# Performance work log

Measured on AMD Instinct MI355X. Metric: run time of the kernel, lower is better.

Reference implementation:

```python
import jax, jax.numpy as jnp
import numpy as np

B, C, D, H, W = 2, 16, 16, 128, 128
CO = 16            # out_channels
C8 = max(C // 8, 1)  # q/k channel dim in CC_module
EPS = 1e-5


def conv3d(x, w, pad):
    # x: [B,C,D,H,W], w: [O,I,kd,kh,kw]
    return jax.lax.conv_general_dilated(
        x, w, (1, 1, 1), [(p, p) for p in pad],
        dimension_numbers=('NCDHW', 'OIDHW', 'NCDHW'))


def bn5d(x, g, b, m, v):
    # eval-mode BatchNorm3d over channel axis 1
    sh = (1, -1, 1, 1, 1)
    return (x - m.reshape(sh)) * (g / jnp.sqrt(v + EPS)).reshape(sh) + b.reshape(sh)


def cc_attention(x, wq, wk, wv, gamma):
    # Criss-cross attention on one depth slice. x: [B,C,H,W]
    q = jnp.einsum('oc,bchw->bohw', wq, x)   # [B,C8,H,W]
    k = jnp.einsum('oc,bchw->bohw', wk, x)   # [B,C8,H,W]
    v = jnp.einsum('oc,bchw->bohw', wv, x)   # [B,C,H,W]
    Hh = x.shape[2]
    # column (H) attention energies, diagonal masked with -inf (CCNet INF trick)
    eH = jnp.einsum('bchw,bcjw->bhwj', q, k)                 # [B,H,W,H]
    eye = jnp.eye(Hh, dtype=bool)[None, :, None, :]
    eH = jnp.where(eye, -jnp.inf, eH)
    # row (W) attention energies
    eW = jnp.einsum('bchw,bchv->bhwv', q, k)                 # [B,H,W,W]
    att = jax.nn.softmax(jnp.concatenate([eH, eW], axis=-1), axis=-1)
    aH, aW = att[..., :Hh], att[..., Hh:]
    oH = jnp.einsum('bhwj,bcjw->bchw', aH, v)
    oW = jnp.einsum('bhwv,bchv->bchw', aW, v)
    return gamma * (oH + oW) + x


def setup_inputs() -> dict:
    key = jax.random.key(0)
    ks = jax.random.split(key, 12)
    f = lambda k, shp, s=0.05: jax.random.normal(k, shp, jnp.float32) * s
    return {
        'x': jax.random.normal(ks[0], (B, C, D, H, W), jnp.float32),
        # Conv3dBNReLU (k=(1,3,3), p=(0,1,1))
        'w_pre': f(ks[1], (C, C, 1, 3, 3)),
        'bn_pre_g': jnp.ones((C,), jnp.float32),
        'bn_pre_b': jnp.zeros((C,), jnp.float32),
        'bn_pre_m': f(ks[2], (C,)),
        'bn_pre_v': jax.random.uniform(ks[3], (C,), jnp.float32, 0.5, 1.5),
        # CC_module params (1x1 convs as matrices)
        'w_q': f(ks[4], (C8, C), 0.2),
        'w_k': f(ks[5], (C8, C), 0.2),
        'w_v': f(ks[6], (C, C), 0.2),
        'cc_gamma': jnp.asarray(0.1, jnp.float32),
        # gate conv BasicConv3d: C -> 4*CO, k=3,s=1,p=1, conv+BN
        'w_gate': f(ks[7], (4 * CO, C, 3, 3, 3)),
        'bn_g': jnp.ones((4 * CO,), jnp.float32),
        'bn_b': jnp.zeros((4 * CO,), jnp.float32),
        'bn_m': f(ks[8], (4 * CO,)),
        'bn_v': jax.random.uniform(ks[9], (4 * CO,), jnp.float32, 0.5, 1.5),
    }


def reference(x, w_pre, bn_pre_g, bn_pre_b, bn_pre_m, bn_pre_v,
              w_q, w_k, w_v, cc_gamma,
              w_gate, bn_g, bn_b, bn_m, bn_v):
    # Conv3dBNReLU
    x = jax.nn.relu(bn5d(conv3d(x, w_pre, (0, 1, 1)),
                         bn_pre_g, bn_pre_b, bn_pre_m, bn_pre_v))
    # criss-cross attention applied twice per depth slice (j in range(2))
    cc2 = lambda xs: cc_attention(
        cc_attention(xs, w_q, w_k, w_v, cc_gamma), w_q, w_k, w_v, cc_gamma)
    x = jax.vmap(cc2, in_axes=2, out_axes=2)(x)
    # SRU gates: conv to 4*CO channels, BN, split, nonlinearities
    gates = bn5d(conv3d(x, w_gate, (1, 1, 1)), bn_g, bn_b, bn_m, bn_v)
    Wx, ft, rt, X = jnp.split(gates, 4, axis=1)
    Wx = jnp.tanh(Wx)
    ft = jax.nn.sigmoid(ft)
    rt = jax.nn.sigmoid(rt)
    X = jnp.tanh(X)  # act == 'tanh'
    # recurrence over depth axis via scan
    Wx_s, ft_s, rt_s, X_s = (jnp.moveaxis(t, 2, 0) for t in (Wx, ft, rt, X))
    C0 = 1.0 - ft_s[0]                        # first step: Ct = 1 - ft
    h0 = rt_s[0] * C0 + (1.0 - rt_s[0]) * X_s[0]

    def step(Ct, inp):
        wx_, ft_, rt_, x_ = inp
        Ct = ft_ * Ct + (1.0 - ft_) * wx_
        ht = rt_ * Ct + (1.0 - rt_) * x_
        return Ct, ht

    _, hts = jax.lax.scan(step, C0, (Wx_s[1:], ft_s[1:], rt_s[1:], X_s[1:]))
    hts = jnp.concatenate([h0[None], hts], axis=0)  # [D,B,CO,H,W]
    return jnp.moveaxis(hts, 0, 2)                  # [B,CO,D,H,W]
```

## Files before the change

kernel.cpp:

```cpp
#include <hip/hip_runtime.h>
#include <math.h>

namespace {
constexpr int B = 2, C = 16, D = 16, H = 128, W = 128;
constexpr int HW   = H * W;
constexpr int DHW  = D * HW;
constexpr int CDHW = C * DHW;
constexpr float EPSBN = 1e-5f;

constexpr long long OFF_R0  = 0;
constexpr long long OFF_R1  = 8388608;
constexpr long long OFF_K   = 16777216;
constexpr long long OFF_KT  = 17825792;
constexpr long long OFF_QT  = 18874368;
constexpr long long OFF_MST = 19922944;
constexpr long long OFF_SO  = 20447232;
constexpr long long OFF_R2  = 20971520;
constexpr long long OFF_R3  = 29360128;
}

using frag_ab = __attribute__((ext_vector_type(8))) short;
using frag_cd = __attribute__((ext_vector_type(4))) float;

__device__ __forceinline__ unsigned short f2bf(float f) {
  unsigned u = __float_as_uint(f);
  u = (u + 0x7FFF + ((u >> 16) & 1)) >> 16;
  return (unsigned short)u;
}
__device__ __forceinline__ float bf2f(short s) {
  return __uint_as_float(((unsigned)(unsigned short)s) << 16);
}
__device__ __forceinline__ unsigned cvt_pk_bf16(float lo, float hi) {
  unsigned r;
  asm volatile("v_cvt_pk_bf16_f32 %0, %1, %2" : "=v"(r) : "v"(lo), "v"(hi));
  return r;
}

__global__ __launch_bounds__(256) void k_x16(
    const float* __restrict__ x, short* __restrict__ XB0)
{
  const int tid = threadIdx.x;
  const int tile = blockIdx.x, d = blockIdx.y, b = blockIdx.z;
  const int h0 = (tile >> 3) * 16, w0 = (tile & 7) * 16;
  const long long xbase = (long long)b * CDHW + (long long)d * HW;
  const int th = tid >> 4, tw = tid & 15;

  float v[16];
  #pragma unroll
  for (int c = 0; c < 16; ++c)
    v[c] = x[xbase + (long long)c * DHW + (h0 + th) * 128 + (w0 + tw)];

  unsigned pk[8];
  #pragma unroll
  for (int c = 0; c < 8; ++c)
    pk[c] = (unsigned)f2bf(v[2 * c]) | ((unsigned)f2bf(v[2 * c + 1]) << 16);
  short* dst = XB0 + ((long long)(b * D + d) * HW + (h0 + th) * 128 + (w0 + tw)) * 16;
  *(uint4*)(dst)     = make_uint4(pk[0], pk[1], pk[2], pk[3]);
  *(uint4*)(dst + 8) = make_uint4(pk[4], pk[5], pk[6], pk[7]);
}

__global__ __launch_bounds__(256) void k_wp(
    const float* __restrict__ wp, short* __restrict__ WP16)
{
  const int idx = blockIdx.x * 256 + threadIdx.x;
  if (idx >= 2 * 16 * 96) return;
  const int u = idx / 96;
  const int k = idx - u * 96;
  const int ks = k >> 5, rem = k & 31;
  const int t = rem >> 3, c8 = rem & 7;
  const int tap = ks * 4 + t;
  const int half = u >> 4, co = u & 15;
  const int cin = half * 8 + c8;
  float v = (tap < 9) ? wp[co * 144 + cin * 9 + tap] : 0.f;
  WP16[idx] = (short)f2bf(v);
}

__global__ __launch_bounds__(256) void k_conv_pre16(
    const short* __restrict__ XB0, const short* __restrict__ WP16,
    const float* __restrict__ bg, const float* __restrict__ bb,
    const float* __restrict__ bm, const float* __restrict__ bv,
    float* __restrict__ X1)
{
  __shared__ short xls[10 * 132 * 8];
  const int tid = threadIdx.x;
  const int rg = blockIdx.x;
  const int d = blockIdx.y, b = blockIdx.z;
  const int h0 = rg * 8;

  const int lane = tid & 63;
  const int wv   = tid >> 6;
  const int p    = lane & 15;
  const int chunk = lane >> 4;

  const short* xb0 = XB0 + (long long)(b * D + d) * HW * 16;
  const frag_ab zero8 = {0, 0, 0, 0, 0, 0, 0, 0};

  frag_cd acc[2][8];
  #pragma unroll
  for (int r2 = 0; r2 < 2; ++r2)
    #pragma unroll
    for (int pg = 0; pg < 8; ++pg)
      acc[r2][pg] = (frag_cd){0.f, 0.f, 0.f, 0.f};

  int offs[3];
  #pragma unroll
  for (int s = 0; s < 3; ++s) {
    int tap = s * 4 + chunk;
    if (tap > 8) tap = 0;
    const int kh = (tap * 11) >> 5;
    const int kw = tap - kh * 3;
    offs[s] = ((2 * wv + kh) * 132 + p + kw) * 8;
  }

  for (int half = 0; half < 2; ++half) {
    for (int idx = tid; idx < 1320; idx += 256) {
      const int row = idx / 132, col = idx - row * 132;
      const int gh = h0 - 1 + row, gw = col - 1;
      frag_ab v = zero8;
      if (gh >= 0 && gh < H && gw >= 0 && gw < W)
        v = *(const frag_ab*)(xb0 + ((long long)gh * 128 + gw) * 16 + half * 8);
      *(frag_ab*)&xls[idx * 8] = v;
    }
    __syncthreads();

    frag_ab a[3];
    {
      const short* wl = WP16 + ((half << 4) + p) * 96 + chunk * 8;
      #pragma unroll
      for (int s = 0; s < 3; ++s)
        a[s] = *(const frag_ab*)(wl + s * 32);
    }

    #pragma unroll
    for (int s = 0; s < 3; ++s) {
      const frag_ab av = a[s];
      const int base0 = offs[s];
      #pragma unroll
      for (int pg = 0; pg < 8; ++pg) {
        frag_ab b0 = *(const frag_ab*)&xls[base0 + pg * 128];
        acc[0][pg] = __builtin_amdgcn_mfma_f32_16x16x32_bf16(av, b0, acc[0][pg], 0, 0, 0);
        frag_ab b1 = *(const frag_ab*)&xls[base0 + 1056 + pg * 128];
        acc[1][pg] = __builtin_amdgcn_mfma_f32_16x16x32_bf16(av, b1, acc[1][pg], 0, 0, 0);
      }
    }
    __syncthreads();
  }

  float sc4[4], bi4[4];
  #pragma unroll
  for (int reg = 0; reg < 4; ++reg) {
    const int co = chunk * 4 + reg;
    float s = bg[co] * rsqrtf(bv[co] + EPSBN);
    sc4[reg] = s;
    bi4[reg] = bb[co] - bm[co] * s;
  }
  const long long xbase = (long long)b * CDHW + (long long)d * HW;
  #pragma unroll
  for (int r2 = 0; r2 < 2; ++r2) {
    const int row = h0 + 2 * wv + r2;
    #pragma unroll
    for (int pg = 0; pg < 8; ++pg)
      #pragma unroll
      for (int reg = 0; reg < 4; ++reg) {
        const int co = chunk * 4 + reg;
        float v = fmaxf(fmaf(acc[r2][pg][reg], sc4[reg], bi4[reg]), 0.f);
        X1[xbase + (long long)co * DHW + row * 128 + pg * 16 + p] = v;
      }
  }
}

__global__ __launch_bounds__(256) void k_qkv(
    const float* __restrict__ xin, const float* __restrict__ wq,
    const float* __restrict__ wk, const float* __restrict__ wv,
    float* __restrict__ Kp, float* __restrict__ KTp, float* __restrict__ QTp,
    short* __restrict__ Vp16, short* __restrict__ VTp16)
{
  const int tid = threadIdx.x;
  const int tile = blockIdx.x, d = blockIdx.y, b = blockIdx.z;
  const int h0 = (tile >> 3) * 16, w0 = (tile & 7) * 16;
  const int ty = tid >> 4, tx = tid & 15;
  const int h = h0 + ty, w = w0 + tx;

  const float* xb = xin + (long long)b * CDHW + (long long)d * HW + h * 128 + w;
  float xv[16];
  #pragma unroll
  for (int c = 0; c < 16; ++c) xv[c] = xb[(long long)c * DHW];

  float q0 = 0, q1 = 0, k0 = 0, k1 = 0, v[16];
  #pragma unroll
  for (int c = 0; c < 16; ++c) {
    q0 = fmaf(wq[c], xv[c], q0);
    q1 = fmaf(wq[16 + c], xv[c], q1);
    k0 = fmaf(wk[c], xv[c], k0);
    k1 = fmaf(wk[16 + c], xv[c], k1);
  }
  #pragma unroll
  for (int o = 0; o < 16; ++o) {
    float a = 0;
    #pragma unroll
    for (int c = 0; c < 16; ++c) a = fmaf(wv[o * 16 + c], xv[c], a);
    v[o] = a;
  }

  const int sl = b * 16 + d;
  const long long base2 = (long long)(sl * 2) * HW;
  const long long baseV = (long long)(sl * 16) * HW;
  const int hw = h * 128 + w;
  Kp[base2 + hw] = k0;
  Kp[base2 + HW + hw] = k1;
  #pragma unroll
  for (int o = 0; o < 16; ++o)
    Vp16[baseV + (long long)o * HW + hw] = (short)f2bf(v[o]);

  __shared__ float lsk[2][16][17];
  __shared__ float lsq[2][16][17];
  __shared__ float lsv[16][16][17];
  lsk[0][ty][tx] = k0; lsk[1][ty][tx] = k1;
  lsq[0][ty][tx] = q0; lsq[1][ty][tx] = q1;
  #pragma unroll
  for (int o = 0; o < 16; ++o) lsv[o][ty][tx] = v[o];
  __syncthreads();

  const int wh = (w0 + ty) * 128 + (h0 + tx);
  KTp[base2 + wh]      = lsk[0][tx][ty];
  KTp[base2 + HW + wh] = lsk[1][tx][ty];
  QTp[base2 + wh]      = lsq[0][tx][ty];
  QTp[base2 + HW + wh] = lsq[1][tx][ty];
  #pragma unroll
  for (int o = 0; o < 16; ++o)
    VTp16[baseV + (long long)o * HW + wh] = (short)f2bf(lsv[o][tx][ty]);
}

template<bool MASK_INNER>
__global__ __launch_bounds__(256) void k_att_row(
    const float* __restrict__ xin, float* __restrict__ OWn,
    const float* __restrict__ Kp, const short* __restrict__ Vp16,
    float* __restrict__ Sip, const float* __restrict__ wq)
{
  __shared__ float kr2[4][128][2];
  __shared__ float q0l[4][128], q1l[4][128];
  __shared__ __align__(16) short v16[4][16][136];
  const int tid = threadIdx.x;
  const int o0 = blockIdx.x * 4, d = blockIdx.y, b = blockIdx.z;
  const int sl = b * 16 + d;
  const long long base2 = (long long)(sl * 2) * HW;
  const long long baseV = (long long)(sl * 16) * HW;
  const long long baseM = (long long)sl * HW;
  const int hi = tid >> 6;
  const int L  = tid & 63;
  const int p  = L & 15;
  const int chunk = L >> 4;
  const int orow = o0 + hi;
  const long long xbase = (long long)b * CDHW + (long long)d * HW;

  for (int kk = tid; kk < 1024; kk += 256) {
    int col = kk & 127;
    int t = kk >> 7;
    int r2 = t >> 1, o = t & 1;
    kr2[r2][col][o] = Kp[base2 + (long long)o * HW + (o0 + r2) * 128 + col];
  }
  for (int idx = tid; idx < 2048; idx += 256) {
    int v4 = idx & 31;
    int t = idx >> 5;
    int c = t & 15, r2 = t >> 4;
    *(uint2*)&v16[r2][c][v4 * 4] =
        *(const uint2*)&Vp16[baseV + (long long)c * HW + (o0 + r2) * 128 + v4 * 4];
  }
  {
    float q0a = 0.f, q0b = 0.f, q1a = 0.f, q1b = 0.f;
    #pragma unroll
    for (int c = 0; c < 16; ++c) {
      const float w0 = wq[c], w1 = wq[16 + c];
      float xa = xin[xbase + (long long)c * DHW + orow * 128 + L];
      float xb2 = xin[xbase + (long long)c * DHW + orow * 128 + L + 64];
      q0a = fmaf(w0, xa, q0a);  q1a = fmaf(w1, xa, q1a);
      q0b = fmaf(w0, xb2, q0b); q1b = fmaf(w1, xb2, q1b);
    }
    q0l[hi][L] = q0a; q0l[hi][L + 64] = q0b;
    q1l[hi][L] = q1a; q1l[hi][L + 64] = q1b;
  }
  __syncthreads();

  float q0r[8], q1r[8];
  #pragma unroll
  for (int ti = 0; ti < 8; ++ti) {
    q0r[ti] = q0l[hi][ti * 16 + p];
    q1r[ti] = q1l[hi][ti * 16 + p];
  }

  frag_cd acc[8];
  #pragma unroll
  for (int ti = 0; ti < 8; ++ti) acc[ti] = (frag_cd){0.f, 0.f, 0.f, 0.f};
  float ssum[8] = {0.f, 0.f, 0.f, 0.f, 0.f, 0.f, 0.f, 0.f};

  #pragma unroll
  for (int ks = 0; ks < 4; ++ks) {
    const int vb = ks * 32 + chunk * 8;
    float2 kv[8];
    const float* kvp = &kr2[hi][vb][0];
    *(float4*)&kv[0] = *(const float4*)(kvp);
    *(float4*)&kv[2] = *(const float4*)(kvp + 4);
    *(float4*)&kv[4] = *(const float4*)(kvp + 8);
    *(float4*)&kv[6] = *(const float4*)(kvp + 12);
    frag_ab bfrag = *(const frag_ab*)&v16[hi][p][vb];

    #pragma unroll
    for (int ti = 0; ti < 8; ++ti) {
      float pv[8];
      #pragma unroll
      for (int j = 0; j < 8; ++j) {
        float e = fmaf(q0r[ti], kv[j].x, q1r[ti] * kv[j].y);
        pv[j] = __expf(e);
      }
      if constexpr (MASK_INNER) {
        const int dj = ti * 16 + p - vb;
        #pragma unroll
        for (int j = 0; j < 8; ++j)
          if (j == dj) pv[j] = 0.f;
      }
      float lsum = 0.f;
      #pragma unroll
      for (int j = 0; j < 8; ++j) lsum += pv[j];
      ssum[ti] += lsum;

      union { frag_ab f; unsigned u[4]; } cv;
      cv.u[0] = cvt_pk_bf16(pv[0], pv[1]);
      cv.u[1] = cvt_pk_bf16(pv[2], pv[3]);
      cv.u[2] = cvt_pk_bf16(pv[4], pv[5]);
      cv.u[3] = cvt_pk_bf16(pv[6], pv[7]);
      acc[ti] = __builtin_amdgcn_mfma_f32_16x16x32_bf16(cv.f, bfrag, acc[ti], 0, 0, 0);
    }
  }

  #pragma unroll
  for (int ti = 0; ti < 8; ++ti) {
    ssum[ti] += __shfl_xor(ssum[ti], 16);
    ssum[ti] += __shfl_xor(ssum[ti], 32);
  }
  if (L < 16) {
    #pragma unroll
    for (int ti = 0; ti < 8; ++ti)
      Sip[baseM + (ti * 16 + L) * 128 + orow] = ssum[ti];
  }

  float* ob = OWn + ((long long)(b * D + d) * HW + orow * 128) * 16;
  #pragma unroll
  for (int ti = 0; ti < 8; ++ti)
    #pragma unroll
    for (int reg = 0; reg < 4; ++reg)
      ob[(ti * 16 + chunk * 4 + reg) * 16 + p] = acc[ti][reg];
}

template<bool MASK_INNER>
__global__ __launch_bounds__(256) void k_att_col(
    const float* __restrict__ KTp, const float* __restrict__ QTp,
    const short* __restrict__ VTp16, float* __restrict__ OHn,
    float* __restrict__ Sop)
{
  __shared__ float kr2[4][128][2];
  __shared__ __align__(16) short v16[4][16][136];
  const int tid = threadIdx.x;
  const int i0 = blockIdx.x * 4, d = blockIdx.y, b = blockIdx.z;
  const int sl = b * 16 + d;
  const long long base2 = (long long)(sl * 2) * HW;
  const long long baseV = (long long)(sl * 16) * HW;
  const long long baseS = (long long)sl * HW;
  const int hi = tid >> 6;
  const int L  = tid & 63;
  const int p  = L & 15;
  const int chunk = L >> 4;
  const int icol = i0 + hi;

  for (int kk = tid; kk < 1024; kk += 256) {
    int col = kk & 127;
    int t = kk >> 7;
    int r2 = t >> 1, o = t & 1;
    kr2[r2][col][o] = KTp[base2 + (long long)o * HW + (i0 + r2) * 128 + col];
  }
  for (int idx = tid; idx < 2048; idx += 256) {
    int j4 = idx & 31;
    int t = idx >> 5;
    int c = t & 15, r2 = t >> 4;
    *(uint2*)&v16[r2][c][j4 * 4] =
        *(const uint2*)&VTp16[baseV + (long long)c * HW + (i0 + r2) * 128 + j4 * 4];
  }
  __syncthreads();

  float q0r[8], q1r[8];
  #pragma unroll
  for (int ti = 0; ti < 8; ++ti) {
    q0r[ti] = QTp[base2 + icol * 128 + ti * 16 + p];
    q1r[ti] = QTp[base2 + HW + icol * 128 + ti * 16 + p];
  }

  frag_cd acc[8];
  #pragma unroll
  for (int ti = 0; ti < 8; ++ti) acc[ti] = (frag_cd){0.f, 0.f, 0.f, 0.f};
  float ssum[8] = {0.f, 0.f, 0.f, 0.f, 0.f, 0.f, 0.f, 0.f};

  #pragma unroll
  for (int ks = 0; ks < 4; ++ks) {
    const int vb = ks * 32 + chunk * 8;
    float2 kv[8];
    const float* kvp = &kr2[hi][vb][0];
    *(float4*)&kv[0] = *(const float4*)(kvp);
    *(float4*)&kv[2] = *(const float4*)(kvp + 4);
    *(float4*)&kv[4] = *(const float4*)(kvp + 8);
    *(float4*)&kv[6] = *(const float4*)(kvp + 12);
    frag_ab bfrag = *(const frag_ab*)&v16[hi][p][vb];

    #pragma unroll
    for (int ti = 0; ti < 8; ++ti) {
      float pv[8];
      #pragma unroll
      for (int j = 0; j < 8; ++j) {
        float e = fmaf(q0r[ti], kv[j].x, q1r[ti] * kv[j].y);
        pv[j] = __expf(e);
      }
      if constexpr (!MASK_INNER) {
        const int dj = ti * 16 + p - vb;
        #pragma unroll
        for (int j = 0; j < 8; ++j)
          if (j == dj) pv[j] = 0.f;
      }
      float lsum = 0.f;
      #pragma unroll
      for (int j = 0; j < 8; ++j) lsum += pv[j];
      ssum[ti] += lsum;

      union { frag_ab f; unsigned u[4]; } cv;
      cv.u[0] = cvt_pk_bf16(pv[0], pv[1]);
      cv.u[1] = cvt_pk_bf16(pv[2], pv[3]);
      cv.u[2] = cvt_pk_bf16(pv[4], pv[5]);
      cv.u[3] = cvt_pk_bf16(pv[6], pv[7]);
      acc[ti] = __builtin_amdgcn_mfma_f32_16x16x32_bf16(cv.f, bfrag, acc[ti], 0, 0, 0);
    }
  }

  #pragma unroll
  for (int ti = 0; ti < 8; ++ti) {
    ssum[ti] += __shfl_xor(ssum[ti], 16);
    ssum[ti] += __shfl_xor(ssum[ti], 32);
  }
  if (L < 16) {
    #pragma unroll
    for (int ti = 0; ti < 8; ++ti)
      Sop[baseS + icol * 128 + ti * 16 + L] = ssum[ti];
  }

  float* ob = OHn + ((long long)(b * D + d) * HW + icol * 128) * 16;
  #pragma unroll
  for (int ti = 0; ti < 8; ++ti)
    #pragma unroll
    for (int reg = 0; reg < 4; ++reg)
      ob[(ti * 16 + chunk * 4 + reg) * 16 + p] = acc[ti][reg];
}

template<bool TO_BF16>
__global__ __launch_bounds__(256) void k_comb(
    const float* __restrict__ Xn, const float* __restrict__ OWn,
    const float* __restrict__ OHn, const float* __restrict__ Sip,
    const float* __restrict__ Sop, const float* __restrict__ gp,
    float* __restrict__ Yt, short* __restrict__ Xb16)
{
  __shared__ float xs[16][16][17], ows[16][16][17];
  const int tid = threadIdx.x;
  const int tile = blockIdx.x, d = blockIdx.y, b = blockIdx.z;
  const int o0 = (tile >> 3) * 16, i0 = (tile & 7) * 16;
  const int sl = b * 16 + d;
  const long long baseM = (long long)sl * HW;
  const long long xbase = (long long)b * CDHW + (long long)d * HW;

  const int to = tid >> 4, ti = tid & 15;
  #pragma unroll
  for (int c = 0; c < 16; ++c) {
    const long long src = xbase + (long long)c * DHW + (o0 + to) * 128 + (i0 + ti);
    xs[c][to][ti] = Xn[src];
  }
  {
    const float* osrc = OWn + ((long long)(b * D + d) * HW + (o0 + to) * 128 + (i0 + ti)) * 16;
    float4 f0 = *(const float4*)(osrc);
    float4 f1 = *(const float4*)(osrc + 4);
    float4 f2 = *(const float4*)(osrc + 8);
    float4 f3 = *(const float4*)(osrc + 12);
    ows[0][to][ti] = f0.x;  ows[1][to][ti] = f0.y;
    ows[2][to][ti] = f0.z;  ows[3][to][ti] = f0.w;
    ows[4][to][ti] = f1.x;  ows[5][to][ti] = f1.y;
    ows[6][to][ti] = f1.z;  ows[7][to][ti] = f1.w;
    ows[8][to][ti] = f2.x;  ows[9][to][ti] = f2.y;
    ows[10][to][ti] = f2.z; ows[11][to][ti] = f2.w;
    ows[12][to][ti] = f3.x; ows[13][to][ti] = f3.y;
    ows[14][to][ti] = f3.z; ows[15][to][ti] = f3.w;
  }
  __syncthreads();

  const int ti2 = tid >> 4, to2 = tid & 15;
  const int i = i0 + ti2, o = o0 + to2;
  const float si = Sip[baseM + i * 128 + o];
  const float so = Sop[baseM + i * 128 + o];
  const float gi = gp[0] / (si + so);

  float oh[16];
  {
    const float* osrc = OHn + ((long long)(b * D + d) * HW + i * 128 + o) * 16;
    float4 f0 = *(const float4*)(osrc);
    float4 f1 = *(const float4*)(osrc + 4);
    float4 f2 = *(const float4*)(osrc + 8);
    float4 f3 = *(const float4*)(osrc + 12);
    oh[0] = f0.x;  oh[1] = f0.y;  oh[2] = f0.z;  oh[3] = f0.w;
    oh[4] = f1.x;  oh[5] = f1.y;  oh[6] = f1.z;  oh[7] = f1.w;
    oh[8] = f2.x;  oh[9] = f2.y;  oh[10] = f2.z; oh[11] = f2.w;
    oh[12] = f3.x; oh[13] = f3.y; oh[14] = f3.z; oh[15] = f3.w;
  }

  float res[16];
  #pragma unroll
  for (int c = 0; c < 16; ++c)
    res[c] = fmaf(gi, ows[c][to2][ti2] + oh[c], xs[c][to2][ti2]);

  if constexpr (!TO_BF16) {
    #pragma unroll
    for (int c = 0; c < 16; ++c)
      Yt[xbase + (long long)c * DHW + i * 128 + o] = res[c];
  } else {
    unsigned pk[8];
    #pragma unroll
    for (int c = 0; c < 8; ++c)
      pk[c] = (unsigned)f2bf(res[2 * c]) | ((unsigned)f2bf(res[2 * c + 1]) << 16);
    short* dst = Xb16 + ((long long)(b * D + d) * HW + i * 128 + o) * 16;
    *(uint4*)(dst)     = make_uint4(pk[0], pk[1], pk[2], pk[3]);
    *(uint4*)(dst + 8) = make_uint4(pk[4], pk[5], pk[6], pk[7]);
  }
}

__global__ __launch_bounds__(256) void k_wt(
    const float* __restrict__ wg, short* __restrict__ WT16)
{
  const int idx = blockIdx.x * 256 + threadIdx.x;
  if (idx >= 2 * 64 * 224) return;
  const int u = idx / 224;
  const int k = idx - u * 224;
  const int ks = k >> 5, rem = k & 31;
  const int t = rem >> 3, c8 = rem & 7;
  const int tap = ks * 4 + t;
  const int half = u >> 6, co = u & 63;
  const int cin = half * 8 + c8;
  float v = (tap < 27) ? wg[co * 432 + cin * 27 + tap] : 0.f;
  WT16[idx] = (short)f2bf(v);
}

__global__ __launch_bounds__(256, 2) void k_gates(
    const short* __restrict__ XB16, const short* __restrict__ WT16,
    short* __restrict__ g0, short* __restrict__ g1,
    short* __restrict__ g2, short* __restrict__ g3)
{
  __shared__ short xls[1584 * 8];
  const int tid = threadIdx.x;
  const int rp = blockIdx.x;
  const int d = blockIdx.y, b = blockIdx.z;
  const int h0 = rp * 2;

  const int lane = tid & 63;
  const int og   = tid >> 6;
  const int p    = lane & 15;
  const int chunk = lane >> 4;

  const short* xb = XB16 + (long long)(b * D) * HW * 16;
  const frag_ab zero8 = {0, 0, 0, 0, 0, 0, 0, 0};

  frag_cd acc[2][8];
  #pragma unroll
  for (int r2 = 0; r2 < 2; ++r2)
    #pragma unroll
    for (int pg = 0; pg < 8; ++pg)
      acc[r2][pg] = (frag_cd){0.f, 0.f, 0.f, 0.f};

  int offs[7];
  #pragma unroll
  for (int s = 0; s < 7; ++s) {
    int tap = s * 4 + chunk;
    if (tap > 26) tap = 0;
    const int kd = (tap * 57) >> 9;
    const int rem = tap - kd * 9;
    const int kh = (rem * 11) >> 5;
    const int kw = rem - kh * 3;
    offs[s] = ((kd * 4 + kh) * 132 + p + kw) * 8;
  }

  for (int half = 0; half < 2; ++half) {
    for (int idx = tid; idx < 1584; idx += 256) {
      const int kd = idx / 528;
      const int rem = idx - kd * 528;
      const int rr = rem / 132;
      const int col = rem - rr * 132;
      const int dd = d - 1 + kd, gh = h0 - 1 + rr, gw = col - 1;
      frag_ab v = zero8;
      if (dd >= 0 && dd < D && gh >= 0 && gh < H && gw >= 0 && gw < W)
        v = *(const frag_ab*)(xb + ((long long)dd * HW + gh * W + gw) * 16 + half * 8);
      *(frag_ab*)&xls[idx * 8] = v;
    }
    __syncthreads();

    frag_ab a[7];
    {
      const short* wl = WT16 + ((half << 6) + og * 16 + p) * 224 + chunk * 8;
      #pragma unroll
      for (int s = 0; s < 7; ++s)
        a[s] = *(const frag_ab*)(wl + s * 32);
    }

    #pragma unroll
    for (int s = 0; s < 7; ++s) {
      const frag_ab av = a[s];
      const int base0 = offs[s];
      #pragma unroll
      for (int pg = 0; pg < 8; ++pg) {
        frag_ab b0 = *(const frag_ab*)&xls[base0 + pg * 128];
        acc[0][pg] = __builtin_amdgcn_mfma_f32_16x16x32_bf16(av, b0, acc[0][pg], 0, 0, 0);
        frag_ab b1 = *(const frag_ab*)&xls[base0 + 1056 + pg * 128];
        acc[1][pg] = __builtin_amdgcn_mfma_f32_16x16x32_bf16(av, b1, acc[1][pg], 0, 0, 0);
      }
    }
    __syncthreads();
  }

  short* gbuf = (og == 0) ? g0 : (og == 1) ? g1 : (og == 2) ? g2 : g3;
  const long long base = (long long)b * CDHW + (long long)d * HW + h0 * W;
  #pragma unroll
  for (int r2 = 0; r2 < 2; ++r2)
    #pragma unroll
    for (int pg = 0; pg < 8; ++pg)
      #pragma unroll
      for (int reg = 0; reg < 4; ++reg) {
        const int cc = chunk * 4 + reg;
        gbuf[base + (long long)cc * DHW + r2 * W + pg * 16 + p] =
            (short)f2bf(acc[r2][pg][reg]);
      }
}

__global__ __launch_bounds__(256) void k_scan(
    const short* __restrict__ g0, const short* __restrict__ g1,
    const short* __restrict__ g2, const short* __restrict__ g3,
    const float* __restrict__ bg, const float* __restrict__ bb,
    const float* __restrict__ bm, const float* __restrict__ bv,
    float* __restrict__ out)
{
  const int g = blockIdx.x * 256 + threadIdx.x;
  const int hw = g & 16383;
  const int cc = (g >> 14) & 15;
  const int b  = g >> 18;

  float sc[4], bi[4];
  #pragma unroll
  for (int gg = 0; gg < 4; ++gg) {
    int ch = gg * 16 + cc;
    float s = bg[ch] * rsqrtf(bv[ch] + EPSBN);
    sc[gg] = s;
    bi[gg] = bb[ch] - bm[ch] * s;
  }

  const long long base = (long long)b * CDHW + (long long)cc * DHW + hw;
  float Ct = 0.f;
  for (int d = 0; d < D; ++d) {
    const long long idx = base + (long long)d * HW;
    float wx = tanhf(fmaf(bf2f(g0[idx]), sc[0], bi[0]));
    float ft = 1.f / (1.f + __expf(-fmaf(bf2f(g1[idx]), sc[1], bi[1])));
    float rt = 1.f / (1.f + __expf(-fmaf(bf2f(g2[idx]), sc[2], bi[2])));
    float xg = tanhf(fmaf(bf2f(g3[idx]), sc[3], bi[3]));
    Ct = (d == 0) ? (1.f - ft) : fmaf(ft, Ct, (1.f - ft) * wx);
    out[idx] = fmaf(rt, Ct, (1.f - rt) * xg);
  }
}

extern "C" void kernel_launch(void* const* d_in, const int* in_sizes, int n_in,
                              void* d_out, int out_size, void* d_ws, size_t ws_size,
                              hipStream_t stream) {
  const float* x      = (const float*)d_in[0];
  const float* w_pre  = (const float*)d_in[1];
  const float* bnpg   = (const float*)d_in[2];
  const float* bnpb   = (const float*)d_in[3];
  const float* bnpm   = (const float*)d_in[4];
  const float* bnpv   = (const float*)d_in[5];
  const float* wq     = (const float*)d_in[6];
  const float* wk     = (const float*)d_in[7];
  const float* wv     = (const float*)d_in[8];
  const float* gamma  = (const float*)d_in[9];
  const float* w_gate = (const float*)d_in[10];
  const float* bng    = (const float*)d_in[11];
  const float* bnb    = (const float*)d_in[12];
  const float* bnm    = (const float*)d_in[13];
  const float* bnv    = (const float*)d_in[14];

  float* ws  = (float*)d_ws;
  float* R0  = ws + OFF_R0;
  float* R1  = ws + OFF_R1;
  float* Kb  = ws + OFF_K;
  float* KTb = ws + OFF_KT;
  float* QTb = ws + OFF_QT;
  float* SI  = ws + OFF_MST;
  float* SO  = ws + OFF_SO;
  float* R2  = ws + OFF_R2;
  float* R3  = ws + OFF_R3;
  short* XB0  = (short*)(ws + OFF_R1);
  short* XB16 = (short*)(ws + OFF_R1);
  short* WP16 = (short*)(ws + OFF_SO);
  short* WT16 = (short*)(ws + OFF_K);
  short* V1b  = (short*)(ws + OFF_R2);
  short* VT1b = (short*)(ws + OFF_R3);
  short* V2b  = (short*)(ws + OFF_R0);
  short* VT2b = (short*)(ws + OFF_R1) + 8388608;
  short* G0b = (short*)(ws + OFF_R0);
  short* G1b = (short*)(ws + OFF_R0) + 8388608;
  short* G2b = (short*)(ws + OFF_R2);
  short* G3b = (short*)(ws + OFF_R2) + 8388608;
  float* out = (float*)d_out;

  const dim3 gTile(64, D, B), gAtt(32, D, B);

  k_wp <<<dim3(12),  dim3(256), 0, stream>>>(w_pre, WP16);
  k_x16<<<gTile,     dim3(256), 0, stream>>>(x, XB0);
  k_conv_pre16<<<dim3(16, D, B), dim3(256), 0, stream>>>(
      XB0, WP16, bnpg, bnpb, bnpm, bnpv, R0);

  k_qkv<<<gTile, dim3(256), 0, stream>>>(R0, wq, wk, wv, Kb, KTb, QTb, V1b, VT1b);
  k_att_row<false><<<gAtt, dim3(256), 0, stream>>>(R0, R1, Kb, V1b, SI, wq);
  k_att_col<false><<<gAtt, dim3(256), 0, stream>>>(KTb, QTb, VT1b, R2, SO);
  k_comb<false><<<gTile, dim3(256), 0, stream>>>(R0, R1, R2, SI, SO, gamma, R3, nullptr);

  k_qkv<<<gTile, dim3(256), 0, stream>>>(R3, wq, wk, wv, Kb, KTb, QTb, V2b, VT2b);
  k_att_row<true><<<gAtt, dim3(256), 0, stream>>>(R3, R2, Kb, V2b, SI, wq);
  k_att_col<true><<<gAtt, dim3(256), 0, stream>>>(KTb, QTb, VT2b, R0, SO);
  k_comb<true><<<gTile, dim3(256), 0, stream>>>(R3, R2, R0, SI, SO, gamma, nullptr, XB16);

  k_wt<<<dim3(112), dim3(256), 0, stream>>>(w_gate, WT16);

  k_gates<<<dim3(64, D, B), dim3(256), 0, stream>>>(XB16, WT16, G0b, G1b, G2b, G3b);

  k_scan<<<dim3(2048), dim3(256), 0, stream>>>(G0b, G1b, G2b, G3b, bng, bnb, bnm, bnv, out);
}
```

Measured before the change: 297.8 us.

## Store attention outputs as bf16 and fuse first combine with second QKV projection

Row and column attention outputs are now written as bf16 instead of fp32, halving those intermediate buffers' traffic. The first combine kernel also computes the q/k/v projections and their transposed copies for the second criss-cross pass, which removes one launch and one full re-read of the intermediate activation. Workspace aliasing is reshuffled to fit the new buffers. The cost is extra bf16 rounding on attention outputs and more registers and shared memory in the fused kernel.

```diff
diff --git a/kernel.cpp b/kernel.cpp
--- a/kernel.cpp
+++ b/kernel.cpp
@@ -233,7 +233,7 @@
 
 template<bool MASK_INNER>
 __global__ __launch_bounds__(256) void k_att_row(
-    const float* __restrict__ xin, float* __restrict__ OWn,
+    const float* __restrict__ xin, short* __restrict__ OWn16,
     const float* __restrict__ Kp, const short* __restrict__ Vp16,
     float* __restrict__ Sip, const float* __restrict__ wq)
 {
@@ -343,18 +343,18 @@
       Sip[baseM + (ti * 16 + L) * 128 + orow] = ssum[ti];
   }
 
-  float* ob = OWn + ((long long)(b * D + d) * HW + orow * 128) * 16;
+  short* ob = OWn16 + ((long long)(b * D + d) * HW + orow * 128) * 16;
   #pragma unroll
   for (int ti = 0; ti < 8; ++ti)
     #pragma unroll
     for (int reg = 0; reg < 4; ++reg)
-      ob[(ti * 16 + chunk * 4 + reg) * 16 + p] = acc[ti][reg];
+      ob[(ti * 16 + chunk * 4 + reg) * 16 + p] = (short)f2bf(acc[ti][reg]);
 }
 
 template<bool MASK_INNER>
 __global__ __launch_bounds__(256) void k_att_col(
     const float* __restrict__ KTp, const float* __restrict__ QTp,
-    const short* __restrict__ VTp16, float* __restrict__ OHn,
+    const short* __restrict__ VTp16, short* __restrict__ OHn16,
     float* __restrict__ Sop)
 {
   __shared__ float kr2[4][128][2];
@@ -448,20 +448,130 @@
       Sop[baseS + icol * 128 + ti * 16 + L] = ssum[ti];
   }
 
-  float* ob = OHn + ((long long)(b * D + d) * HW + icol * 128) * 16;
+  short* ob = OHn16 + ((long long)(b * D + d) * HW + icol * 128) * 16;
   #pragma unroll
   for (int ti = 0; ti < 8; ++ti)
     #pragma unroll
     for (int reg = 0; reg < 4; ++reg)
-      ob[(ti * 16 + chunk * 4 + reg) * 16 + p] = acc[ti][reg];
-}
-
-template<bool TO_BF16>
-__global__ __launch_bounds__(256) void k_comb(
-    const float* __restrict__ Xn, const float* __restrict__ OWn,
-    const float* __restrict__ OHn, const float* __restrict__ Sip,
+      ob[(ti * 16 + chunk * 4 + reg) * 16 + p] = (short)f2bf(acc[ti][reg]);
+}
+
+__global__ __launch_bounds__(256) void k_comb_qkv(
+    const float* __restrict__ Xn, const short* __restrict__ OWn16,
+    const short* __restrict__ OHn16, const float* __restrict__ Sip,
     const float* __restrict__ Sop, const float* __restrict__ gp,
-    float* __restrict__ Yt, short* __restrict__ Xb16)
+    const float* __restrict__ wq, const float* __restrict__ wk,
+    const float* __restrict__ wv,
+    float* __restrict__ Yt, float* __restrict__ Kp, float* __restrict__ KTp,
+    float* __restrict__ QTp, short* __restrict__ Vp16, short* __restrict__ VTp16)
+{
+  __shared__ float xs[16][16][17];
+  __shared__ float ows[16][16][17];
+  __shared__ float lsk[2][16][17], lsq[2][16][17];
+  const int tid = threadIdx.x;
+  const int tile = blockIdx.x, d = blockIdx.y, b = blockIdx.z;
+  const int o0 = (tile >> 3) * 16, i0 = (tile & 7) * 16;
+  const int sl = b * 16 + d;
+  const long long baseM = (long long)sl * HW;
+  const long long base2 = (long long)(sl * 2) * HW;
+  const long long baseV = (long long)(sl * 16) * HW;
+  const long long xbase = (long long)b * CDHW + (long long)d * HW;
+
+  const int to = tid >> 4, ti = tid & 15;
+  #pragma unroll
+  for (int c = 0; c < 16; ++c) {
+    const long long src = xbase + (long long)c * DHW + (o0 + to) * 128 + (i0 + ti);
+    xs[c][to][ti] = Xn[src];
+  }
+  {
+    const short* osrc = OWn16 + ((long long)(b * D + d) * HW + (o0 + to) * 128 + (i0 + ti)) * 16;
+    frag_ab f0 = *(const frag_ab*)(osrc);
+    frag_ab f1 = *(const frag_ab*)(osrc + 8);
+    #pragma unroll
+    for (int c = 0; c < 8; ++c) {
+      ows[c][to][ti]     = bf2f(f0[c]);
+      ows[c + 8][to][ti] = bf2f(f1[c]);
+    }
+  }
+  __syncthreads();
+
+  const int ti2 = tid >> 4, to2 = tid & 15;
+  const int i = i0 + ti2, o = o0 + to2;
+  const float si = Sip[baseM + i * 128 + o];
+  const float so = Sop[baseM + i * 128 + o];
+  const float gi = gp[0] / (si + so);
+
+  float oh[16];
+  {
+    const short* osrc = OHn16 + ((long long)(b * D + d) * HW + i * 128 + o) * 16;
+    frag_ab f0 = *(const frag_ab*)(osrc);
+    frag_ab f1 = *(const frag_ab*)(osrc + 8);
+    #pragma unroll
+    for (int c = 0; c < 8; ++c) { oh[c] = bf2f(f0[c]); oh[c + 8] = bf2f(f1[c]); }
+  }
+
+  float res[16];
+  #pragma unroll
+  for (int c = 0; c < 16; ++c)
+    res[c] = fmaf(gi, ows[c][to2][ti2] + oh[c], xs[c][to2][ti2]);
+
+  #pragma unroll
+  for (int c = 0; c < 16; ++c)
+    Yt[xbase + (long long)c * DHW + i * 128 + o] = res[c];
+
+  float q0 = 0, q1 = 0, k0 = 0, k1 = 0, v[16];
+  #pragma unroll
+  for (int c = 0; c < 16; ++c) {
+    q0 = fmaf(wq[c], res[c], q0);
+    q1 = fmaf(wq[16 + c], res[c], q1);
+    k0 = fmaf(wk[c], res[c], k0);
+    k1 = fmaf(wk[16 + c], res[c], k1);
+  }
+  #pragma unroll
+  for (int oo = 0; oo < 16; ++oo) {
+    float a = 0;
+    #pragma unroll
+    for (int c = 0; c < 16; ++c) a = fmaf(wv[oo * 16 + c], res[c], a);
+    v[oo] = a;
+  }
+
+  const int hw = i * 128 + o;
+  Kp[base2 + hw] = k0;
+  Kp[base2 + HW + hw] = k1;
+  #pragma unroll
+  for (int oo = 0; oo < 16; ++oo)
+    Vp16[baseV + (long long)oo * HW + hw] = (short)f2bf(v[oo]);
+
+  lsk[0][to2][ti2] = k0; lsk[1][to2][ti2] = k1;
+  lsq[0][to2][ti2] = q0; lsq[1][to2][ti2] = q1;
+  __syncthreads();
+
+  #pragma unroll
+  for (int c = 0; c < 16; ++c) xs[c][to2][ti2] = v[c];
+
+  {
+    const int a = tid >> 4, bb2 = tid & 15;
+    const long long wh = (long long)(o0 + a) * 128 + (i0 + bb2);
+    KTp[base2 + wh]      = lsk[0][a][bb2];
+    KTp[base2 + HW + wh] = lsk[1][a][bb2];
+    QTp[base2 + wh]      = lsq[0][a][bb2];
+    QTp[base2 + HW + wh] = lsq[1][a][bb2];
+  }
+  __syncthreads();
+  {
+    const int a = tid >> 4, bb2 = tid & 15;
+    const long long wh = (long long)(o0 + a) * 128 + (i0 + bb2);
+    #pragma unroll
+    for (int c = 0; c < 16; ++c)
+      VTp16[baseV + (long long)c * HW + wh] = (short)f2bf(xs[c][a][bb2]);
+  }
+}
+
+__global__ __launch_bounds__(256) void k_comb_bf(
+    const float* __restrict__ Xn, const short* __restrict__ OWn16,
+    const short* __restrict__ OHn16, const float* __restrict__ Sip,
+    const float* __restrict__ Sop, const float* __restrict__ gp,
+    short* __restrict__ Xb16)
 {
   __shared__ float xs[16][16][17], ows[16][16][17];
   const int tid = threadIdx.x;
@@ -478,19 +588,14 @@
     xs[c][to][ti] = Xn[src];
   }
   {
-    const float* osrc = OWn + ((long long)(b * D + d) * HW + (o0 + to) * 128 + (i0 + ti)) * 16;
-    float4 f0 = *(const float4*)(osrc);
-    float4 f1 = *(const float4*)(osrc + 4);
-    float4 f2 = *(const float4*)(osrc + 8);
-    float4 f3 = *(const float4*)(osrc + 12);
-    ows[0][to][ti] = f0.x;  ows[1][to][ti] = f0.y;
-    ows[2][to][ti] = f0.z;  ows[3][to][ti] = f0.w;
-    ows[4][to][ti] = f1.x;  ows[5][to][ti] = f1.y;
-    ows[6][to][ti] = f1.z;  ows[7][to][ti] = f1.w;
-    ows[8][to][ti] = f2.x;  ows[9][to][ti] = f2.y;
-    ows[10][to][ti] = f2.z; ows[11][to][ti] = f2.w;
-    ows[12][to][ti] = f3.x; ows[13][to][ti] = f3.y;
-    ows[14][to][ti] = f3.z; ows[15][to][ti] = f3.w;
+    const short* osrc = OWn16 + ((long long)(b * D + d) * HW + (o0 + to) * 128 + (i0 + ti)) * 16;
+    frag_ab f0 = *(const frag_ab*)(osrc);
+    frag_ab f1 = *(const frag_ab*)(osrc + 8);
+    #pragma unroll
+    for (int c = 0; c < 8; ++c) {
+      ows[c][to][ti]     = bf2f(f0[c]);
+      ows[c + 8][to][ti] = bf2f(f1[c]);
+    }
   }
   __syncthreads();
 
@@ -502,15 +607,11 @@
 
   float oh[16];
   {
-    const float* osrc = OHn + ((long long)(b * D + d) * HW + i * 128 + o) * 16;
-    float4 f0 = *(const float4*)(osrc);
-    float4 f1 = *(const float4*)(osrc + 4);
-    float4 f2 = *(const float4*)(osrc + 8);
-    float4 f3 = *(const float4*)(osrc + 12);
-    oh[0] = f0.x;  oh[1] = f0.y;  oh[2] = f0.z;  oh[3] = f0.w;
-    oh[4] = f1.x;  oh[5] = f1.y;  oh[6] = f1.z;  oh[7] = f1.w;
-    oh[8] = f2.x;  oh[9] = f2.y;  oh[10] = f2.z; oh[11] = f2.w;
-    oh[12] = f3.x; oh[13] = f3.y; oh[14] = f3.z; oh[15] = f3.w;
+    const short* osrc = OHn16 + ((long long)(b * D + d) * HW + i * 128 + o) * 16;
+    frag_ab f0 = *(const frag_ab*)(osrc);
+    frag_ab f1 = *(const frag_ab*)(osrc + 8);
+    #pragma unroll
+    for (int c = 0; c < 8; ++c) { oh[c] = bf2f(f0[c]); oh[c + 8] = bf2f(f1[c]); }
   }
 
   float res[16];
@@ -518,19 +619,13 @@
   for (int c = 0; c < 16; ++c)
     res[c] = fmaf(gi, ows[c][to2][ti2] + oh[c], xs[c][to2][ti2]);
 
-  if constexpr (!TO_BF16) {
-    #pragma unroll
-    for (int c = 0; c < 16; ++c)
-      Yt[xbase + (long long)c * DHW + i * 128 + o] = res[c];
-  } else {
-    unsigned pk[8];
-    #pragma unroll
-    for (int c = 0; c < 8; ++c)
-      pk[c] = (unsigned)f2bf(res[2 * c]) | ((unsigned)f2bf(res[2 * c + 1]) << 16);
-    short* dst = Xb16 + ((long long)(b * D + d) * HW + i * 128 + o) * 16;
-    *(uint4*)(dst)     = make_uint4(pk[0], pk[1], pk[2], pk[3]);
-    *(uint4*)(dst + 8) = make_uint4(pk[4], pk[5], pk[6], pk[7]);
-  }
+  unsigned pk[8];
+  #pragma unroll
+  for (int c = 0; c < 8; ++c)
+    pk[c] = (unsigned)f2bf(res[2 * c]) | ((unsigned)f2bf(res[2 * c + 1]) << 16);
+  short* dst = Xb16 + ((long long)(b * D + d) * HW + i * 128 + o) * 16;
+  *(uint4*)(dst)     = make_uint4(pk[0], pk[1], pk[2], pk[3]);
+  *(uint4*)(dst + 8) = make_uint4(pk[4], pk[5], pk[6], pk[7]);
 }
 
 __global__ __launch_bounds__(256) void k_wt(
@@ -693,22 +788,25 @@
 
   float* ws  = (float*)d_ws;
   float* R0  = ws + OFF_R0;
-  float* R1  = ws + OFF_R1;
+  float* R3  = ws + OFF_R3;
   float* Kb  = ws + OFF_K;
   float* KTb = ws + OFF_KT;
   float* QTb = ws + OFF_QT;
   float* SI  = ws + OFF_MST;
   float* SO  = ws + OFF_SO;
-  float* R2  = ws + OFF_R2;
-  float* R3  = ws + OFF_R3;
-  short* XB0  = (short*)(ws + OFF_R1);
-  short* XB16 = (short*)(ws + OFF_R1);
-  short* WP16 = (short*)(ws + OFF_SO);
-  short* WT16 = (short*)(ws + OFF_K);
-  short* V1b  = (short*)(ws + OFF_R2);
-  short* VT1b = (short*)(ws + OFF_R3);
-  short* V2b  = (short*)(ws + OFF_R0);
-  short* VT2b = (short*)(ws + OFF_R1) + 8388608;
+
+  short* XB0   = (short*)(ws + OFF_R1);
+  short* WP16  = (short*)(ws + OFF_SO);
+  short* WT16  = (short*)(ws + OFF_K);
+  short* V1b   = (short*)(ws + OFF_R2);
+  short* VT1b  = (short*)(ws + OFF_R3);
+  short* OW1   = (short*)(ws + OFF_R1);
+  short* OH1   = (short*)(ws + OFF_R2);
+  short* V2b   = (short*)(ws + OFF_R2) + 8388608;
+  short* VT2b  = (short*)(ws + OFF_R1) + 8388608;
+  short* OW2   = (short*)(ws + OFF_R0);
+  short* OH2   = (short*)(ws + OFF_R2);
+  short* XB16  = (short*)(ws + OFF_R1);
   short* G0b = (short*)(ws + OFF_R0);
   short* G1b = (short*)(ws + OFF_R0) + 8388608;
   short* G2b = (short*)(ws + OFF_R2);
@@ -723,14 +821,15 @@
       XB0, WP16, bnpg, bnpb, bnpm, bnpv, R0);
 
   k_qkv<<<gTile, dim3(256), 0, stream>>>(R0, wq, wk, wv, Kb, KTb, QTb, V1b, VT1b);
-  k_att_row<false><<<gAtt, dim3(256), 0, stream>>>(R0, R1, Kb, V1b, SI, wq);
-  k_att_col<false><<<gAtt, dim3(256), 0, stream>>>(KTb, QTb, VT1b, R2, SO);
-  k_comb<false><<<gTile, dim3(256), 0, stream>>>(R0, R1, R2, SI, SO, gamma, R3, nullptr);
-
-  k_qkv<<<gTile, dim3(256), 0, stream>>>(R3, wq, wk, wv, Kb, KTb, QTb, V2b, VT2b);
-  k_att_row<true><<<gAtt, dim3(256), 0, stream>>>(R3, R2, Kb, V2b, SI, wq);
-  k_att_col<true><<<gAtt, dim3(256), 0, stream>>>(KTb, QTb, VT2b, R0, SO);
-  k_comb<true><<<gTile, dim3(256), 0, stream>>>(R3, R2, R0, SI, SO, gamma, nullptr, XB16);
+  k_att_row<false><<<gAtt, dim3(256), 0, stream>>>(R0, OW1, Kb, V1b, SI, wq);
+  k_att_col<false><<<gAtt, dim3(256), 0, stream>>>(KTb, QTb, VT1b, OH1, SO);
+  k_comb_qkv<<<gTile, dim3(256), 0, stream>>>(
+      R0, OW1, OH1, SI, SO, gamma, wq, wk, wv,
+      R3, Kb, KTb, QTb, V2b, VT2b);
+
+  k_att_row<true><<<gAtt, dim3(256), 0, stream>>>(R3, OW2, Kb, V2b, SI, wq);
+  k_att_col<true><<<gAtt, dim3(256), 0, stream>>>(KTb, QTb, VT2b, OH2, SO);
+  k_comb_bf<<<gTile, dim3(256), 0, stream>>>(R3, OW2, OH2, SI, SO, gamma, XB16);
 
   k_wt<<<dim3(112), dim3(256), 0, stream>>>(w_gate, WT16);
 
```

New measurement: 281.5 us, median of 2. 1.06x faster.
